# Kernel optimization log

Measured on AMD Instinct MI355X. Metric: run time of the kernel, lower is better.

Reference implementation:

```python
import jax, jax.numpy as jnp
import numpy as np

D = 4096  # input_size
H = 4096  # hidden_size


def setup_inputs() -> dict:
    key = jax.random.key(0)
    ks = jax.random.split(key, 18)
    inp = {
        "x": jax.random.normal(ks[0], (D,), jnp.float32),
        "h_prev": jax.random.normal(ks[1], (H,), jnp.float32),
        "c_prev": jax.random.normal(ks[2], (H, H), jnp.float32),
        "n_prev": jax.random.normal(ks[3], (H,), jnp.float32),
        "m_prev": jax.random.normal(ks[4], (H,), jnp.float32),
    }
    names = ["q", "k", "v", "i", "f", "o"]
    for idx, nm in enumerate(names):
        inp[f"W{nm}"] = jax.random.normal(ks[5 + 2 * idx], (H, D), jnp.float32) * 0.02
        inp[f"b{nm}"] = jax.random.normal(ks[6 + 2 * idx], (H,), jnp.float32) * 0.02
    return inp


def reference(x, h_prev, c_prev, n_prev, m_prev,
              Wq, bq, Wk, bk, Wv, bv, Wi, bi, Wf, bf, Wo, bo):
    # Six linear projections (nn.Linear: W @ x + b for 1-D x)
    q = Wq @ x + bq
    k = (Wk @ x + bk) / jnp.sqrt(jnp.float32(H))
    v = Wv @ x + bv
    o = jax.nn.sigmoid(Wo @ x + bo)
    i_tilde = Wi @ x + bi
    f_tilde = Wf @ x + bf

    # Stabilizer state and exp gates
    m_t = jnp.maximum(f_tilde + m_prev, i_tilde)          # [H]
    i_g = jnp.exp(i_tilde - m_t)                          # [H]
    f_g = jnp.exp(f_tilde + m_prev - m_t)                 # [H]

    # Rank-1 outer-product state update; gates broadcast over last axis (as in torch)
    c_t = f_g * c_prev + i_g * jnp.outer(v, k)            # [H, H]
    n_t = f_g * n_prev + i_g * k                          # [H]

    # Normalized matvec output
    denom = jnp.maximum(jnp.abs(jnp.dot(n_t, q)), jnp.float32(1.0))
    h_t = o * (c_t @ q) / denom                           # [H]
    return (h_t, c_t, n_t, m_t)
```

## Files before the change

### kernel.cpp

```cpp
#include <hip/hip_runtime.h>
#include <math.h>

#define HD 4096

__device__ __forceinline__ float row_dot(const float* __restrict__ W,
                                         const float4* __restrict__ xs4,
                                         int row, int lane) {
    const float4* Wrow = (const float4*)(W + (size_t)row * HD);
    float acc = 0.f;
#pragma unroll
    for (int t = 0; t < 16; ++t) {
        float4 w  = Wrow[t * 64 + lane];
        float4 xv = xs4[t * 64 + lane];
        acc += w.x * xv.x + w.y * xv.y + w.z * xv.z + w.w * xv.w;
    }
#pragma unroll
    for (int off = 32; off > 0; off >>= 1)
        acc += __shfl_xor(acc, off, 64);
    return acc;
}

__global__ __launch_bounds__(256) void k_gemv6(
    const float* __restrict__ x,
    const float* __restrict__ n_prev, const float* __restrict__ m_prev,
    const float* __restrict__ Wq, const float* __restrict__ bq,
    const float* __restrict__ Wk, const float* __restrict__ bk,
    const float* __restrict__ Wv, const float* __restrict__ bv,
    const float* __restrict__ Wi, const float* __restrict__ bi,
    const float* __restrict__ Wf, const float* __restrict__ bf,
    const float* __restrict__ Wo, const float* __restrict__ bo,
    float* __restrict__ ws_q, float* __restrict__ ws_v,
    float* __restrict__ ws_o, float* __restrict__ ws_fg,
    float* __restrict__ ws_ik,
    float* __restrict__ out_n, float* __restrict__ out_m)
{
    __shared__ float xs[HD];
    const int tid = threadIdx.x;
    {
        const float4* x4  = (const float4*)x;
        float4*       xs4 = (float4*)xs;
        for (int i = tid; i < HD / 4; i += 256) xs4[i] = x4[i];
    }
    __syncthreads();

    const int wave = tid >> 6;
    const int lane = tid & 63;
    const int row  = blockIdx.x * 4 + wave;
    const float4* xs4 = (const float4*)xs;

    float dq = row_dot(Wq, xs4, row, lane);
    float dk = row_dot(Wk, xs4, row, lane);
    float dv = row_dot(Wv, xs4, row, lane);
    float di = row_dot(Wi, xs4, row, lane);
    float df = row_dot(Wf, xs4, row, lane);
    float dо = row_dot(Wo, xs4, row, lane);

    if (lane == 0) {
        float q  = dq + bq[row];
        float k  = (dk + bk[row]) * (1.0f / 64.0f);
        float v  = dv + bv[row];
        float it = di + bi[row];
        float ft = df + bf[row];
        float o  = 1.0f / (1.0f + expf(-(dо + bo[row])));
        float mp = m_prev[row];
        float mt = fmaxf(ft + mp, it);
        float ig = expf(it - mt);
        float fg = expf(ft + mp - mt);
        float nt = fg * n_prev[row] + ig * k;
        ws_q[row]  = q;
        ws_v[row]  = v;
        ws_o[row]  = o;
        ws_fg[row] = fg;
        ws_ik[row] = ig * k;
        out_n[row] = nt;
        out_m[row] = mt;
    }
}

__global__ __launch_bounds__(256) void k_denom(
    const float* __restrict__ out_n, const float* __restrict__ ws_q,
    float* __restrict__ denom)
{
    const int tid = threadIdx.x;
    float acc = 0.f;
    for (int i = tid; i < HD; i += 256) acc += out_n[i] * ws_q[i];
#pragma unroll
    for (int off = 32; off > 0; off >>= 1) acc += __shfl_xor(acc, off, 64);
    __shared__ float red[4];
    if ((tid & 63) == 0) red[tid >> 6] = acc;
    __syncthreads();
    if (tid == 0) {
        float s = red[0] + red[1] + red[2] + red[3];
        denom[0] = fmaxf(fabsf(s), 1.0f);
    }
}

__global__ __launch_bounds__(256) void k_ct(
    const float* __restrict__ c_prev,
    const float* __restrict__ ws_q, const float* __restrict__ ws_v,
    const float* __restrict__ ws_o, const float* __restrict__ ws_fg,
    const float* __restrict__ ws_ik, const float* __restrict__ denom,
    float* __restrict__ out_h, float* __restrict__ out_c)
{
    const int row = blockIdx.x;
    const int tid = threadIdx.x;
    const float vr = ws_v[row];

    const float4* cp4 = (const float4*)(c_prev + (size_t)row * HD);
    float4*       ct4 = (float4*)(out_c + (size_t)row * HD);
    const float4* fg4 = (const float4*)ws_fg;
    const float4* ik4 = (const float4*)ws_ik;
    const float4* q4  = (const float4*)ws_q;

    float acc = 0.f;
#pragma unroll
    for (int t = 0; t < 4; ++t) {
        const int idx = t * 256 + tid;
        float4 c  = cp4[idx];
        float4 f  = fg4[idx];
        float4 ik = ik4[idx];
        float4 qq = q4[idx];
        float4 ct;
        ct.x = f.x * c.x + ik.x * vr;
        ct.y = f.y * c.y + ik.y * vr;
        ct.z = f.z * c.z + ik.z * vr;
        ct.w = f.w * c.w + ik.w * vr;
        ct4[idx] = ct;
        acc += ct.x * qq.x + ct.y * qq.y + ct.z * qq.z + ct.w * qq.w;
    }
#pragma unroll
    for (int off = 32; off > 0; off >>= 1) acc += __shfl_xor(acc, off, 64);
    __shared__ float red[4];
    if ((tid & 63) == 0) red[tid >> 6] = acc;
    __syncthreads();
    if (tid == 0) {
        float s = red[0] + red[1] + red[2] + red[3];
        out_h[row] = ws_o[row] * s / denom[0];
    }
}

extern "C" void kernel_launch(void* const* d_in, const int* in_sizes, int n_in,
                              void* d_out, int out_size, void* d_ws, size_t ws_size,
                              hipStream_t stream) {
    const float* x      = (const float*)d_in[0];
    const float* c_prev = (const float*)d_in[2];
    const float* n_prev = (const float*)d_in[3];
    const float* m_prev = (const float*)d_in[4];
    const float* Wq = (const float*)d_in[5];  const float* bq = (const float*)d_in[6];
    const float* Wk = (const float*)d_in[7];  const float* bk = (const float*)d_in[8];
    const float* Wv = (const float*)d_in[9];  const float* bv = (const float*)d_in[10];
    const float* Wi = (const float*)d_in[11]; const float* bi = (const float*)d_in[12];
    const float* Wf = (const float*)d_in[13]; const float* bf = (const float*)d_in[14];
    const float* Wo = (const float*)d_in[15]; const float* bo = (const float*)d_in[16];

    float* out   = (float*)d_out;
    float* out_h = out;
    float* out_c = out + HD;
    float* out_n = out + HD + (size_t)HD * HD;
    float* out_m = out_n + HD;

    float* ws    = (float*)d_ws;
    float* ws_q  = ws;
    float* ws_v  = ws + 1 * HD;
    float* ws_o  = ws + 2 * HD;
    float* ws_fg = ws + 3 * HD;
    float* ws_ik = ws + 4 * HD;
    float* denom = ws + 5 * HD;

    k_gemv6<<<HD / 4, 256, 0, stream>>>(x, n_prev, m_prev,
                                        Wq, bq, Wk, bk, Wv, bv,
                                        Wi, bi, Wf, bf, Wo, bo,
                                        ws_q, ws_v, ws_o, ws_fg, ws_ik,
                                        out_n, out_m);
    k_denom<<<1, 256, 0, stream>>>(out_n, ws_q, denom);
    k_ct<<<HD, 256, 0, stream>>>(c_prev, ws_q, ws_v, ws_o, ws_fg, ws_ik,
                                 denom, out_h, out_c);
}
```

Baseline: 435.3 us.

## Split GEMV across matrices, move gates to separate kernel, fuse denom reduction

The six-matrix GEMV now launches one block per (matrix, 4-row group), giving six times more blocks, and writes raw dot products to a workspace. A small gates kernel applies the biases and nonlinearities and also computes per-block partial sums of n·q, which replaces the single-block denom kernel. The ct kernel sums the 16 partials itself and issues all of its loads before computing. The extra parallelism should hide memory latency in the weight-bound GEMV. In exchange the dot products make an extra round trip through global memory.

```diff
diff --git a/kernel.cpp b/kernel.cpp
--- a/kernel.cpp
+++ b/kernel.cpp
@@ -3,103 +3,113 @@
 
 #define HD 4096
 
-__device__ __forceinline__ float row_dot(const float* __restrict__ W,
-                                         const float4* __restrict__ xs4,
-                                         int row, int lane) {
-    const float4* Wrow = (const float4*)(W + (size_t)row * HD);
-    float acc = 0.f;
-#pragma unroll
-    for (int t = 0; t < 16; ++t) {
-        float4 w  = Wrow[t * 64 + lane];
-        float4 xv = xs4[t * 64 + lane];
-        acc += w.x * xv.x + w.y * xv.y + w.z * xv.z + w.w * xv.w;
-    }
-#pragma unroll
-    for (int off = 32; off > 0; off >>= 1)
-        acc += __shfl_xor(acc, off, 64);
-    return acc;
-}
-
-__global__ __launch_bounds__(256) void k_gemv6(
+__global__ __launch_bounds__(256, 6) void k_gemv(
     const float* __restrict__ x,
-    const float* __restrict__ n_prev, const float* __restrict__ m_prev,
-    const float* __restrict__ Wq, const float* __restrict__ bq,
-    const float* __restrict__ Wk, const float* __restrict__ bk,
-    const float* __restrict__ Wv, const float* __restrict__ bv,
-    const float* __restrict__ Wi, const float* __restrict__ bi,
-    const float* __restrict__ Wf, const float* __restrict__ bf,
-    const float* __restrict__ Wo, const float* __restrict__ bo,
-    float* __restrict__ ws_q, float* __restrict__ ws_v,
-    float* __restrict__ ws_o, float* __restrict__ ws_fg,
-    float* __restrict__ ws_ik,
-    float* __restrict__ out_n, float* __restrict__ out_m)
+    const float* __restrict__ Wq, const float* __restrict__ Wk,
+    const float* __restrict__ Wv, const float* __restrict__ Wi,
+    const float* __restrict__ Wf, const float* __restrict__ Wo,
+    float* __restrict__ ws_dots)
 {
     __shared__ float xs[HD];
     const int tid = threadIdx.x;
     {
         const float4* x4  = (const float4*)x;
-        float4*       xs4 = (float4*)xs;
-        for (int i = tid; i < HD / 4; i += 256) xs4[i] = x4[i];
+        float4*       sx4 = (float4*)xs;
+#pragma unroll
+        for (int i = 0; i < 4; ++i) sx4[i * 256 + tid] = x4[i * 256 + tid];
     }
     __syncthreads();
 
     const int wave = tid >> 6;
     const int lane = tid & 63;
-    const int row  = blockIdx.x * 4 + wave;
-    const float4* xs4 = (const float4*)xs;
+    const int mat  = blockIdx.x >> 10;
+    const int row  = ((blockIdx.x & 1023) << 2) | wave;
 
-    float dq = row_dot(Wq, xs4, row, lane);
-    float dk = row_dot(Wk, xs4, row, lane);
-    float dv = row_dot(Wv, xs4, row, lane);
-    float di = row_dot(Wi, xs4, row, lane);
-    float df = row_dot(Wf, xs4, row, lane);
-    float dо = row_dot(Wo, xs4, row, lane);
+    const float* W = Wq;
+    if      (mat == 1) W = Wk;
+    else if (mat == 2) W = Wv;
+    else if (mat == 3) W = Wi;
+    else if (mat == 4) W = Wf;
+    else if (mat == 5) W = Wo;
 
-    if (lane == 0) {
-        float q  = dq + bq[row];
-        float k  = (dk + bk[row]) * (1.0f / 64.0f);
-        float v  = dv + bv[row];
-        float it = di + bi[row];
-        float ft = df + bf[row];
-        float o  = 1.0f / (1.0f + expf(-(dо + bo[row])));
-        float mp = m_prev[row];
-        float mt = fmaxf(ft + mp, it);
-        float ig = expf(it - mt);
-        float fg = expf(ft + mp - mt);
-        float nt = fg * n_prev[row] + ig * k;
-        ws_q[row]  = q;
-        ws_v[row]  = v;
-        ws_o[row]  = o;
-        ws_fg[row] = fg;
-        ws_ik[row] = ig * k;
-        out_n[row] = nt;
-        out_m[row] = mt;
+    const float4* Wrow = (const float4*)(W + (size_t)row * HD) + lane;
+    const float4* sx4  = (const float4*)xs + lane;
+
+    float a0 = 0.f, a1 = 0.f;
+#pragma unroll
+    for (int t = 0; t < 16; t += 2) {
+        float4 w0 = Wrow[t * 64];
+        float4 x0 = sx4[t * 64];
+        float4 w1 = Wrow[(t + 1) * 64];
+        float4 x1 = sx4[(t + 1) * 64];
+        a0 += w0.x * x0.x + w0.y * x0.y + w0.z * x0.z + w0.w * x0.w;
+        a1 += w1.x * x1.x + w1.y * x1.y + w1.z * x1.z + w1.w * x1.w;
     }
+    float acc = a0 + a1;
+#pragma unroll
+    for (int off = 32; off > 0; off >>= 1)
+        acc += __shfl_xor(acc, off, 64);
+
+    if (lane == 0) ws_dots[(mat << 12) | row] = acc;
 }
 
-__global__ __launch_bounds__(256) void k_denom(
-    const float* __restrict__ out_n, const float* __restrict__ ws_q,
-    float* __restrict__ denom)
+__global__ __launch_bounds__(256) void k_gates(
+    const float* __restrict__ ws_dots,
+    const float* __restrict__ bq, const float* __restrict__ bk,
+    const float* __restrict__ bv, const float* __restrict__ bi,
+    const float* __restrict__ bf, const float* __restrict__ bo,
+    const float* __restrict__ n_prev, const float* __restrict__ m_prev,
+    float* __restrict__ ws_q, float* __restrict__ ws_v,
+    float* __restrict__ ws_o, float* __restrict__ ws_fg,
+    float* __restrict__ ws_ik,
+    float* __restrict__ out_n, float* __restrict__ out_m,
+    float* __restrict__ ws_nq)
 {
     const int tid = threadIdx.x;
-    float acc = 0.f;
-    for (int i = tid; i < HD; i += 256) acc += out_n[i] * ws_q[i];
+    const int row = blockIdx.x * 256 + tid;
+
+    float dq  = ws_dots[0 * HD + row];
+    float dk  = ws_dots[1 * HD + row];
+    float dv  = ws_dots[2 * HD + row];
+    float di  = ws_dots[3 * HD + row];
+    float df  = ws_dots[4 * HD + row];
+    float d_o = ws_dots[5 * HD + row];
+
+    float q  = dq + bq[row];
+    float k  = (dk + bk[row]) * (1.0f / 64.0f);
+    float v  = dv + bv[row];
+    float o  = 1.0f / (1.0f + expf(-(d_o + bo[row])));
+    float it = di + bi[row];
+    float ft = df + bf[row];
+    float mp = m_prev[row];
+    float mt = fmaxf(ft + mp, it);
+    float ig = expf(it - mt);
+    float fg = expf(ft + mp - mt);
+    float nt = fg * n_prev[row] + ig * k;
+
+    ws_q[row]  = q;
+    ws_v[row]  = v;
+    ws_o[row]  = o;
+    ws_fg[row] = fg;
+    ws_ik[row] = ig * k;
+    out_n[row] = nt;
+    out_m[row] = mt;
+
+    float acc = nt * q;
 #pragma unroll
-    for (int off = 32; off > 0; off >>= 1) acc += __shfl_xor(acc, off, 64);
+    for (int off = 32; off > 0; off >>= 1)
+        acc += __shfl_xor(acc, off, 64);
     __shared__ float red[4];
     if ((tid & 63) == 0) red[tid >> 6] = acc;
     __syncthreads();
-    if (tid == 0) {
-        float s = red[0] + red[1] + red[2] + red[3];
-        denom[0] = fmaxf(fabsf(s), 1.0f);
-    }
+    if (tid == 0) ws_nq[blockIdx.x] = red[0] + red[1] + red[2] + red[3];
 }
 
 __global__ __launch_bounds__(256) void k_ct(
     const float* __restrict__ c_prev,
     const float* __restrict__ ws_q, const float* __restrict__ ws_v,
     const float* __restrict__ ws_o, const float* __restrict__ ws_fg,
-    const float* __restrict__ ws_ik, const float* __restrict__ denom,
+    const float* __restrict__ ws_ik, const float* __restrict__ ws_nq,
     float* __restrict__ out_h, float* __restrict__ out_c)
 {
     const int row = blockIdx.x;
@@ -112,30 +122,41 @@
     const float4* ik4 = (const float4*)ws_ik;
     const float4* q4  = (const float4*)ws_q;
 
+    float4 c[4], f[4], k[4], qv[4];
+#pragma unroll
+    for (int t = 0; t < 4; ++t) {
+        const int idx = t * 256 + tid;
+        c[t]  = cp4[idx];
+        f[t]  = fg4[idx];
+        k[t]  = ik4[idx];
+        qv[t] = q4[idx];
+    }
+
     float acc = 0.f;
 #pragma unroll
     for (int t = 0; t < 4; ++t) {
         const int idx = t * 256 + tid;
-        float4 c  = cp4[idx];
-        float4 f  = fg4[idx];
-        float4 ik = ik4[idx];
-        float4 qq = q4[idx];
         float4 ct;
-        ct.x = f.x * c.x + ik.x * vr;
-        ct.y = f.y * c.y + ik.y * vr;
-        ct.z = f.z * c.z + ik.z * vr;
-        ct.w = f.w * c.w + ik.w * vr;
+        ct.x = f[t].x * c[t].x + k[t].x * vr;
+        ct.y = f[t].y * c[t].y + k[t].y * vr;
+        ct.z = f[t].z * c[t].z + k[t].z * vr;
+        ct.w = f[t].w * c[t].w + k[t].w * vr;
         ct4[idx] = ct;
-        acc += ct.x * qq.x + ct.y * qq.y + ct.z * qq.z + ct.w * qq.w;
+        acc += ct.x * qv[t].x + ct.y * qv[t].y + ct.z * qv[t].z + ct.w * qv[t].w;
     }
 #pragma unroll
-    for (int off = 32; off > 0; off >>= 1) acc += __shfl_xor(acc, off, 64);
+    for (int off = 32; off > 0; off >>= 1)
+        acc += __shfl_xor(acc, off, 64);
     __shared__ float red[4];
     if ((tid & 63) == 0) red[tid >> 6] = acc;
     __syncthreads();
     if (tid == 0) {
         float s = red[0] + red[1] + red[2] + red[3];
-        out_h[row] = ws_o[row] * s / denom[0];
+        float d = 0.f;
+#pragma unroll
+        for (int i = 0; i < 16; ++i) d += ws_nq[i];
+        float den = fmaxf(fabsf(d), 1.0f);
+        out_h[row] = ws_o[row] * s / den;
     }
 }
 
@@ -159,20 +180,20 @@
     float* out_n = out + HD + (size_t)HD * HD;
     float* out_m = out_n + HD;
 
-    float* ws    = (float*)d_ws;
-    float* ws_q  = ws;
-    float* ws_v  = ws + 1 * HD;
-    float* ws_o  = ws + 2 * HD;
-    float* ws_fg = ws + 3 * HD;
-    float* ws_ik = ws + 4 * HD;
-    float* denom = ws + 5 * HD;
+    float* ws      = (float*)d_ws;
+    float* ws_dots = ws;
+    float* ws_q    = ws + 6 * HD;
+    float* ws_v    = ws + 7 * HD;
+    float* ws_o    = ws + 8 * HD;
+    float* ws_fg   = ws + 9 * HD;
+    float* ws_ik   = ws + 10 * HD;
+    float* ws_nq   = ws + 11 * HD;
 
-    k_gemv6<<<HD / 4, 256, 0, stream>>>(x, n_prev, m_prev,
-                                        Wq, bq, Wk, bk, Wv, bv,
-                                        Wi, bi, Wf, bf, Wo, bo,
-                                        ws_q, ws_v, ws_o, ws_fg, ws_ik,
-                                        out_n, out_m);
-    k_denom<<<1, 256, 0, stream>>>(out_n, ws_q, denom);
+    k_gemv<<<6 * 1024, 256, 0, stream>>>(x, Wq, Wk, Wv, Wi, Wf, Wo, ws_dots);
+    k_gates<<<16, 256, 0, stream>>>(ws_dots, bq, bk, bv, bi, bf, bo,
+                                    n_prev, m_prev,
+                                    ws_q, ws_v, ws_o, ws_fg, ws_ik,
+                                    out_n, out_m, ws_nq);
     k_ct<<<HD, 256, 0, stream>>>(c_prev, ws_q, ws_v, ws_o, ws_fg, ws_ik,
-                                 denom, out_h, out_c);
+                                 ws_nq, out_h, out_c);
 }
```

Measured after the change: 437.1 us. Within noise of the previous version (+0.4%).
